# Kernel tuning notes

Measured on AMD Instinct MI355X. Metric: run time of the kernel, lower is better.

Reference implementation:

```python
import jax, jax.numpy as jnp
import numpy as np

N_NODES = 100000
N_EDGES = 1600000
N_GRAPHS = 100
DIMS = [128, 128, 118, 103, 5]  # in_feats, h, h-10, h-25, num_classes


def setup_inputs() -> dict:
    key = jax.random.key(0)
    ks = jax.random.split(key, 16)
    inp = {
        "in_feat": jax.random.normal(ks[0], (N_NODES, DIMS[0]), dtype=jnp.float32),
        "src": jax.random.randint(ks[1], (N_EDGES,), 0, N_NODES, dtype=jnp.int32),
        "dst": jax.random.randint(ks[2], (N_EDGES,), 0, N_NODES, dtype=jnp.int32),
        "graph_ids": (jnp.arange(N_NODES, dtype=jnp.int32) // (N_NODES // N_GRAPHS)),
    }
    # SAGEConv params: fc_self (no bias), fc_neigh (no bias), shared bias
    for l in range(4):
        din, dout = DIMS[l], DIMS[l + 1]
        inp[f"ws{l+1}"] = jax.random.normal(ks[3 + 3 * l], (din, dout), dtype=jnp.float32) * 0.05
        inp[f"wn{l+1}"] = jax.random.normal(ks[4 + 3 * l], (din, dout), dtype=jnp.float32) * 0.05
        inp[f"b{l+1}"] = jnp.zeros((dout,), dtype=jnp.float32)
    return inp


def reference(in_feat, src, dst, graph_ids,
              ws1, wn1, b1, ws2, wn2, b2, ws3, wn3, b3, ws4, wn4, b4):
    N = in_feat.shape[0]
    # in-degree per dst node, clamped to 1 (DGL: degs.clamp(min=1))
    deg = jnp.clip(jax.ops.segment_sum(jnp.ones((src.shape[0],), in_feat.dtype), dst,
                                       num_segments=N), 1.0, None)

    def sage(h, ws, wn, b):
        # mean-aggregate neighbor features: gather over src, scatter-add to dst
        agg = jax.ops.segment_sum(h[src], dst, num_segments=N) / deg[:, None]
        return h @ ws + agg @ wn + b

    h = jax.nn.relu(sage(in_feat, ws1, wn1, b1))
    h = jax.nn.relu(sage(h, ws2, wn2, b2))
    h = jax.nn.relu(sage(h, ws3, wn3, b3))
    h = sage(h, ws4, wn4, b4)

    # dgl.mean_nodes: per-graph mean pooling over nodes
    ones = jnp.ones((N,), h.dtype)
    cnt = jax.ops.segment_sum(ones, graph_ids, num_segments=N_GRAPHS)
    pooled = jax.ops.segment_sum(h, graph_ids, num_segments=N_GRAPHS) / cnt[:, None]
    return pooled
```

## Files before the change

### kernel.cpp

```cpp
#include <hip/hip_runtime.h>
#include <cstdint>
#include <cstddef>

typedef unsigned int uint32;
typedef unsigned short ushort16;
typedef __attribute__((ext_vector_type(8))) short short8;
typedef __attribute__((ext_vector_type(4))) float floatx4;

__device__ __forceinline__ ushort16 f2bf(float f) {
    uint32 u = __builtin_bit_cast(uint32, f);
    uint32 r = (u + 0x7fffu + ((u >> 16) & 1u)) >> 16;
    return (ushort16)r;
}
__device__ __forceinline__ float bf2f(ushort16 h) {
    uint32 u = ((uint32)h) << 16;
    return __builtin_bit_cast(float, u);
}

#define PBS 4096

__global__ __launch_bounds__(256) void bucket_hist_kernel(
    const int* __restrict__ dst, int* __restrict__ bcnt, int E, int NBUCK) {
    __shared__ int l[512];
    int t = threadIdx.x;
    for (int b = t; b < NBUCK; b += 256) l[b] = 0;
    __syncthreads();
    int e0 = blockIdx.x * PBS;
    int e1 = e0 + PBS; if (e1 > E) e1 = E;
    for (int j = e0 + t; j < e1; j += 256)
        atomicAdd(&l[dst[j] >> 8], 1);
    __syncthreads();
    for (int b = t; b < NBUCK; b += 256) {
        int c = l[b];
        if (c) atomicAdd(&bcnt[b], c);
    }
}

__global__ __launch_bounds__(256) void bucket_scan_kernel(
    const int* __restrict__ bcnt, int* __restrict__ bucketOff,
    int* __restrict__ cursorA, int NBUCK, int E) {
    __shared__ int a[512], b[512];
    int t = threadIdx.x;
    a[t] = (t < NBUCK) ? bcnt[t] : 0;
    a[t + 256] = (t + 256 < NBUCK) ? bcnt[t + 256] : 0;
    __syncthreads();
    int* cur = a; int* nxt = b;
    for (int o = 1; o < 512; o <<= 1) {
#pragma unroll
        for (int i = t; i < 512; i += 256)
            nxt[i] = cur[i] + ((i >= o) ? cur[i - o] : 0);
        __syncthreads();
        int* tmp = cur; cur = nxt; nxt = tmp;
    }
#pragma unroll
    for (int i = t; i < 512; i += 256) {
        if (i < NBUCK) {
            int off = (i == 0) ? 0 : cur[i - 1];
            bucketOff[i] = off;
            cursorA[i] = off;
        }
    }
    if (t == 0) bucketOff[NBUCK] = E;
}

__global__ __launch_bounds__(256) void bucket_partition_kernel(
    const int* __restrict__ src, const int* __restrict__ dst,
    int* __restrict__ cursorA, uint32* __restrict__ ebuf, int E, int NBUCK) {
    __shared__ int lbase[512];
    int tid = threadIdx.x;
    for (int b = tid; b < NBUCK; b += 256) lbase[b] = 0;
    __syncthreads();
    int e0 = blockIdx.x * PBS;
    int e1 = e0 + PBS; if (e1 > E) e1 = E;
    for (int j = e0 + tid; j < e1; j += 256)
        atomicAdd(&lbase[dst[j] >> 8], 1);
    __syncthreads();
    for (int b = tid; b < NBUCK; b += 256) {
        int c = lbase[b];
        lbase[b] = c ? atomicAdd(&cursorA[b], c) : 0;
    }
    __syncthreads();
    for (int j = e0 + tid; j < e1; j += 256) {
        int d = dst[j];
        int p = atomicAdd(&lbase[d >> 8], 1);
        ebuf[p] = ((uint32)src[j] << 8) | (uint32)(d & 255);
    }
}

__global__ __launch_bounds__(256) void bucket_build_kernel(
    const uint32* __restrict__ ebuf, const int* __restrict__ bucketOff,
    int* __restrict__ row_ptr, float* __restrict__ degf,
    int* __restrict__ csr, int N, int E) {
    __shared__ int ldeg[256];
    __shared__ int lscan[256];
    __shared__ int lcur[256];
    int b = blockIdx.x, t = threadIdx.x;
    int n0 = b << 8;
    int s = bucketOff[b], e = bucketOff[b + 1];
    ldeg[t] = 0;
    __syncthreads();
    for (int j = s + t; j < e; j += 256)
        atomicAdd(&ldeg[ebuf[j] & 255u], 1);
    __syncthreads();
    int v = ldeg[t];
    lscan[t] = v;
    __syncthreads();
    for (int off = 1; off < 256; off <<= 1) {
        int x = (t >= off) ? lscan[t - off] : 0;
        __syncthreads();
        lscan[t] += x;
        __syncthreads();
    }
    int excl = lscan[t] - v;
    int node = n0 + t;
    if (node < N) {
        row_ptr[node] = s + excl;
        degf[node] = (float)(v > 0 ? v : 1);
    }
    lcur[t] = s + excl;
    __syncthreads();
    for (int j = s + t; j < e; j += 256) {
        uint32 en = ebuf[j];
        int p = atomicAdd(&lcur[en & 255u], 1);
        csr[p] = (int)(en >> 8);
    }
    if (b == 0 && t == 0) row_ptr[N] = E;
}

__global__ void conv_bf16_kernel(const float* __restrict__ x, ushort16* __restrict__ y, int n8) {
    int i = blockIdx.x * blockDim.x + threadIdx.x;
    if (i >= n8) return;
    const float4 a = *(const float4*)(x + (size_t)i * 8);
    const float4 b = *(const float4*)(x + (size_t)i * 8 + 4);
    uint4 o;
    o.x = (uint32)f2bf(a.x) | ((uint32)f2bf(a.y) << 16);
    o.y = (uint32)f2bf(a.z) | ((uint32)f2bf(a.w) << 16);
    o.z = (uint32)f2bf(b.x) | ((uint32)f2bf(b.y) << 16);
    o.w = (uint32)f2bf(b.z) | ((uint32)f2bf(b.w) << 16);
    *(uint4*)(y + (size_t)i * 8) = o;
}

__global__ void prep_w_all_kernel(
    const float* __restrict__ W0s, const float* __restrict__ W0n,
    const float* __restrict__ W1s, const float* __restrict__ W1n,
    const float* __restrict__ W2s, const float* __restrict__ W2n,
    ushort16* __restrict__ Whi, ushort16* __restrict__ Wlo) {
    int mat = blockIdx.x >> 6;
    int idx = (blockIdx.x & 63) * 256 + threadIdx.x;
    const float* Wt[6] = {W0s, W0n, W1s, W1n, W2s, W2n};
    const int Kt[6] = {128, 128, 128, 128, 118, 118};
    const int Mt[6] = {128, 128, 118, 118, 103, 103};
    int n = idx >> 7, k = idx & 127;
    int K = Kt[mat], M = Mt[mat];
    float w = (k < K && n < M) ? Wt[mat][(size_t)k * M + n] : 0.f;
    ushort16 h = f2bf(w);
    float lo = w - bf2f(h);
    Whi[(size_t)mat * 16384 + idx] = h;
    Wlo[(size_t)mat * 16384 + idx] = f2bf(lo);
}

template<int UNROLL>
__global__ __launch_bounds__(256) void aggregate_pre_kernel(
    const ushort16* __restrict__ h,
    const int* __restrict__ row_ptr, const int* __restrict__ csr,
    const float* __restrict__ degf, ushort16* __restrict__ aggH, int N) {
    int wid = threadIdx.x >> 6;
    int lane = threadIdx.x & 63;
    int node = blockIdx.x * 4 + wid;
    if (node >= N) return;
    int s = row_ptr[node], e = row_ptr[node + 1];
    int c = lane & 15;
    int eo = lane >> 4;
    float aLo[4] = {}, aHi[4] = {};
    int j = s + eo;
    for (; j + (UNROLL - 1) * 4 < e; j += UNROLL * 4) {
        uint4 v[UNROLL];
#pragma unroll
        for (int u = 0; u < UNROLL; ++u) {
            int src_n = csr[j + u * 4];
            v[u] = *(const uint4*)(h + ((size_t)src_n << 7) + (c << 3));
        }
#pragma unroll
        for (int u = 0; u < UNROLL; ++u) {
            uint32 w[4] = {v[u].x, v[u].y, v[u].z, v[u].w};
#pragma unroll
            for (int p = 0; p < 4; ++p) {
                aLo[p] += __builtin_bit_cast(float, w[p] << 16);
                aHi[p] += __builtin_bit_cast(float, w[p] & 0xffff0000u);
            }
        }
    }
    for (; j + 4 < e; j += 8) {
        int s0 = csr[j];
        int s1 = csr[j + 4];
        uint4 v0 = *(const uint4*)(h + ((size_t)s0 << 7) + (c << 3));
        uint4 v1 = *(const uint4*)(h + ((size_t)s1 << 7) + (c << 3));
        uint32 w0[4] = {v0.x, v0.y, v0.z, v0.w};
        uint32 w1[4] = {v1.x, v1.y, v1.z, v1.w};
#pragma unroll
        for (int p = 0; p < 4; ++p) {
            aLo[p] += __builtin_bit_cast(float, w0[p] << 16);
            aHi[p] += __builtin_bit_cast(float, w0[p] & 0xffff0000u);
            aLo[p] += __builtin_bit_cast(float, w1[p] << 16);
            aHi[p] += __builtin_bit_cast(float, w1[p] & 0xffff0000u);
        }
    }
    for (; j < e; j += 4) {
        int src_n = csr[j];
        uint4 v = *(const uint4*)(h + ((size_t)src_n << 7) + (c << 3));
        uint32 w[4] = {v.x, v.y, v.z, v.w};
#pragma unroll
        for (int p = 0; p < 4; ++p) {
            aLo[p] += __builtin_bit_cast(float, w[p] << 16);
            aHi[p] += __builtin_bit_cast(float, w[p] & 0xffff0000u);
        }
    }
#pragma unroll
    for (int m = 16; m < 64; m <<= 1) {
#pragma unroll
        for (int p = 0; p < 4; ++p) {
            aLo[p] += __shfl_xor(aLo[p], m, 64);
            aHi[p] += __shfl_xor(aHi[p], m, 64);
        }
    }
    if (lane < 16) {
        float inv = 1.f / degf[node];
        uint4 ov;
        ov.x = (uint32)f2bf(aLo[0] * inv) | ((uint32)f2bf(aHi[0] * inv) << 16);
        ov.y = (uint32)f2bf(aLo[1] * inv) | ((uint32)f2bf(aHi[1] * inv) << 16);
        ov.z = (uint32)f2bf(aLo[2] * inv) | ((uint32)f2bf(aHi[2] * inv) << 16);
        ov.w = (uint32)f2bf(aLo[3] * inv) | ((uint32)f2bf(aHi[3] * inv) << 16);
        *(uint4*)(aggH + ((size_t)node << 7) + (c << 3)) = ov;
    }
}

#define RS 40
__global__ __launch_bounds__(256) void mfma_fused_kernel(
    const ushort16* __restrict__ A, const ushort16* __restrict__ G,
    const ushort16* __restrict__ Whi, const ushort16* __restrict__ Wlo,
    const float* __restrict__ bias,
    ushort16* __restrict__ Out, int N, int M) {
    __shared__ ushort16 Bs[4][64 * RS];
    const int tid = threadIdx.x;
    const int wave = tid >> 6;
    const int lane = tid & 63;
    const int quad = lane >> 4;
    const int m16 = lane & 15;
    const ushort16* Wg[4] = {Whi, Wlo, Whi + 16384, Wlo + 16384};

    floatx4 acc[4] = {};

    const int n0 = blockIdx.y * 64;
    int rowA = blockIdx.x * 64 + wave * 16 + m16;
    if (rowA >= N) rowA = N - 1;
    const ushort16* Arow = A + (size_t)rowA * 128;
    const ushort16* Grow = G + (size_t)rowA * 128;

    const int sn = tid >> 2, sh = tid & 3;
    for (int k0 = 0; k0 < 128; k0 += 32) {
#pragma unroll
        for (int mat = 0; mat < 4; ++mat) {
            const ushort16* g = Wg[mat] + (size_t)(n0 + sn) * 128 + k0 + sh * 8;
            *(uint4*)(&Bs[mat][sn * RS + sh * 8]) = *(const uint4*)g;
        }
        short8 af = *(const short8*)(Arow + k0 + quad * 8);
        short8 gf = *(const short8*)(Grow + k0 + quad * 8);
        __syncthreads();
#pragma unroll
        for (int t = 0; t < 4; ++t) {
            int nb = t * 16 + m16;
            short8 bsh = *(const short8*)(&Bs[0][nb * RS + quad * 8]);
            short8 bsl = *(const short8*)(&Bs[1][nb * RS + quad * 8]);
            short8 bnh = *(const short8*)(&Bs[2][nb * RS + quad * 8]);
            short8 bnl = *(const short8*)(&Bs[3][nb * RS + quad * 8]);
            acc[t] = __builtin_amdgcn_mfma_f32_16x16x32_bf16(af, bsh, acc[t], 0, 0, 0);
            acc[t] = __builtin_amdgcn_mfma_f32_16x16x32_bf16(gf, bnh, acc[t], 0, 0, 0);
            acc[t] = __builtin_amdgcn_mfma_f32_16x16x32_bf16(af, bsl, acc[t], 0, 0, 0);
            acc[t] = __builtin_amdgcn_mfma_f32_16x16x32_bf16(gf, bnl, acc[t], 0, 0, 0);
        }
        __syncthreads();
    }

    int rowBase = blockIdx.x * 64 + wave * 16 + quad * 4;
#pragma unroll
    for (int t = 0; t < 4; ++t) {
        int colt = n0 + t * 16 + m16;
        bool inc = (colt < M);
        float b = inc ? bias[colt] : 0.f;
#pragma unroll
        for (int r = 0; r < 4; ++r) {
            int row = rowBase + r;
            if (row < N) {
                float v = inc ? fmaxf(acc[t][r] + b, 0.f) : 0.f;
                Out[(size_t)row * 128 + colt] = f2bf(v);
            }
        }
    }
}

__global__ __launch_bounds__(256) void gemm4_kernel(
    const ushort16* __restrict__ A, const float* __restrict__ ws,
    const float* __restrict__ wn, const float* __restrict__ b4,
    float* __restrict__ Cs, float* __restrict__ Cn, int N, int K, int M) {
    __shared__ float Wsh[520], Wnh[520];
    int tid = threadIdx.x;
    for (int i = tid; i < K * M; i += 256) { Wsh[i] = ws[i]; Wnh[i] = wn[i]; }
    __syncthreads();
    int node = blockIdx.x * 256 + tid;
    if (node >= N) return;
    const ushort16* row = A + ((size_t)node << 7);
    float s[5] = {}, n[5] = {};
    for (int c8 = 0; c8 * 8 < K; ++c8) {
        uint4 v = *(const uint4*)(row + c8 * 8);
        uint32 w[4] = {v.x, v.y, v.z, v.w};
#pragma unroll
        for (int j = 0; j < 8; ++j) {
            int k = c8 * 8 + j;
            if (k < K) {
                float a = (j & 1) ? __builtin_bit_cast(float, w[j >> 1] & 0xffff0000u)
                                  : __builtin_bit_cast(float, w[j >> 1] << 16);
#pragma unroll
                for (int m = 0; m < 5; ++m) {
                    s[m] += a * Wsh[k * 5 + m];
                    n[m] += a * Wnh[k * 5 + m];
                }
            }
        }
    }
    size_t o = (size_t)node * 8;
#pragma unroll
    for (int m = 0; m < 5; ++m) {
        Cs[o + m] = s[m] + b4[m];
        Cn[o + m] = n[m];
    }
#pragma unroll
    for (int m = 5; m < 8; ++m) { Cs[o + m] = 0.f; Cn[o + m] = 0.f; }
}

template<int CPW, int UNROLL, int SLOG>
__global__ __launch_bounds__(256) void aggregate_fp32_kernel(
    const float* __restrict__ hs, const float* __restrict__ hn,
    const int* __restrict__ row_ptr, const int* __restrict__ csr,
    const float* __restrict__ degf, float* __restrict__ out, int N) {
    constexpr int EPI = 64 / CPW;
    int wid = threadIdx.x >> 6;
    int lane = threadIdx.x & 63;
    int node = blockIdx.x * 4 + wid;
    if (node >= N) return;
    int s = row_ptr[node], e = row_ptr[node + 1];
    int c = lane & (CPW - 1);
    int eo = lane / CPW;
    float4 acc = make_float4(0.f, 0.f, 0.f, 0.f);
    int j = s + eo;
    for (; j + (UNROLL - 1) * EPI < e; j += UNROLL * EPI) {
        float4 v[UNROLL];
#pragma unroll
        for (int u = 0; u < UNROLL; ++u) {
            int src_n = csr[j + u * EPI];
            v[u] = *(const float4*)(hn + ((size_t)src_n << SLOG) + (c << 2));
        }
#pragma unroll
        for (int u = 0; u < UNROLL; ++u) {
            acc.x += v[u].x; acc.y += v[u].y; acc.z += v[u].z; acc.w += v[u].w;
        }
    }
    for (; j < e; j += EPI) {
        int src_n = csr[j];
        float4 v = *(const float4*)(hn + ((size_t)src_n << SLOG) + (c << 2));
        acc.x += v.x; acc.y += v.y; acc.z += v.z; acc.w += v.w;
    }
#pragma unroll
    for (int m = CPW; m < 64; m <<= 1) {
        acc.x += __shfl_xor(acc.x, m, 64);
        acc.y += __shfl_xor(acc.y, m, 64);
        acc.z += __shfl_xor(acc.z, m, 64);
        acc.w += __shfl_xor(acc.w, m, 64);
    }
    if (lane < CPW) {
        float d = 1.f / degf[node];
        size_t o = ((size_t)node << SLOG) + (lane << 2);
        float4 hv = *(const float4*)(hs + o);
        float4 r;
        r.x = hv.x + acc.x * d;
        r.y = hv.y + acc.y * d;
        r.z = hv.z + acc.z * d;
        r.w = hv.w + acc.w * d;
        *(float4*)(out + o) = r;
    }
}

__global__ __launch_bounds__(256) void pool_kernel(
    const float* __restrict__ h, float* __restrict__ out, int npg) {
    __shared__ float sh[4][5];
    int g = blockIdx.x;
    int t = threadIdx.x;
    float acc[5] = {0.f, 0.f, 0.f, 0.f, 0.f};
    int base = g * npg;
    for (int i = t; i < npg; i += 256) {
        const float* r = h + ((size_t)(base + i) << 3);
#pragma unroll
        for (int f = 0; f < 5; ++f) acc[f] += r[f];
    }
#pragma unroll
    for (int off = 32; off > 0; off >>= 1) {
#pragma unroll
        for (int f = 0; f < 5; ++f) acc[f] += __shfl_down(acc[f], off, 64);
    }
    int wid = t >> 6, lane = t & 63;
    if (lane == 0) {
#pragma unroll
        for (int f = 0; f < 5; ++f) sh[wid][f] = acc[f];
    }
    __syncthreads();
    if (t == 0) {
        float inv = 1.f / (float)npg;
#pragma unroll
        for (int f = 0; f < 5; ++f)
            out[g * 5 + f] = (sh[0][f] + sh[1][f] + sh[2][f] + sh[3][f]) * inv;
    }
}

extern "C" void kernel_launch(void* const* d_in, const int* in_sizes, int n_in,
                              void* d_out, int out_size, void* d_ws, size_t ws_size,
                              hipStream_t stream) {
    const float* in_feat = (const float*)d_in[0];
    const int* src = (const int*)d_in[1];
    const int* dst = (const int*)d_in[2];
    const int DIMS[5] = {128, 128, 118, 103, 5};
    const int N = in_sizes[0] / 128;
    const int E = in_sizes[1];
    const int G = out_size / 5;
    const int NBUCK = (N + 255) >> 8;

    char* base = (char*)d_ws;
    size_t off = 0;
    auto carve = [&](size_t bytes) -> void* {
        off = (off + 255) & ~(size_t)255;
        void* p = base + off;
        off += bytes;
        return p;
    };
    int* bcnt = (int*)carve((size_t)NBUCK * 4);
    int* bucketOff = (int*)carve((size_t)(NBUCK + 1) * 4);
    int* cursorA = (int*)carve((size_t)NBUCK * 4);
    int* row_ptr = (int*)carve((size_t)(N + 1) * 4);
    float* degf = (float*)carve((size_t)N * 4);
    uint32* ebuf = (uint32*)carve((size_t)E * 4);
    int* csr = (int*)carve((size_t)E * 4);
    ushort16* buf0 = (ushort16*)carve((size_t)(N + 256) * 128 * 2);
    ushort16* buf1 = (ushort16*)carve((size_t)(N + 256) * 128 * 2);
    ushort16* aggH = (ushort16*)carve((size_t)(N + 256) * 128 * 2);
    ushort16* Whi = (ushort16*)carve((size_t)6 * 16384 * 2);
    ushort16* Wlo = (ushort16*)carve((size_t)6 * 16384 * 2);
    float* Cs4 = (float*)carve((size_t)N * 8 * 4);
    float* Cn4 = (float*)carve((size_t)N * 8 * 4);
    float* out4 = (float*)carve((size_t)N * 8 * 4);
    (void)n_in; (void)ws_size;

    hipMemsetAsync(bcnt, 0, (size_t)NBUCK * 4, stream);
    bucket_hist_kernel<<<(E + PBS - 1) / PBS, 256, 0, stream>>>(dst, bcnt, E, NBUCK);
    bucket_scan_kernel<<<1, 256, 0, stream>>>(bcnt, bucketOff, cursorA, NBUCK, E);
    bucket_partition_kernel<<<(E + PBS - 1) / PBS, 256, 0, stream>>>(
        src, dst, cursorA, ebuf, E, NBUCK);
    bucket_build_kernel<<<NBUCK, 256, 0, stream>>>(
        ebuf, bucketOff, row_ptr, degf, csr, N, E);

    int n8 = N * 16;
    conv_bf16_kernel<<<(n8 + 255) / 256, 256, 0, stream>>>(in_feat, buf0, n8);
    prep_w_all_kernel<<<6 * 64, 256, 0, stream>>>(
        (const float*)d_in[4], (const float*)d_in[5],
        (const float*)d_in[7], (const float*)d_in[8],
        (const float*)d_in[10], (const float*)d_in[11],
        Whi, Wlo);

    ushort16* hb[4] = {buf0, buf1, buf0, buf1};
    dim3 ggrid((N + 63) / 64, 2);
    for (int l = 0; l < 3; ++l) {
        int M = DIMS[l + 1];
        const float* b = (const float*)d_in[6 + 3 * l];
        aggregate_pre_kernel<4><<<(N + 3) / 4, 256, 0, stream>>>(
            hb[l], row_ptr, csr, degf, aggH, N);
        mfma_fused_kernel<<<ggrid, 256, 0, stream>>>(
            hb[l], aggH, Whi + (size_t)l * 2 * 16384, Wlo + (size_t)l * 2 * 16384,
            b, hb[l + 1], N, M);
    }

    gemm4_kernel<<<(N + 255) / 256, 256, 0, stream>>>(
        hb[3], (const float*)d_in[13], (const float*)d_in[14], (const float*)d_in[15],
        Cs4, Cn4, N, DIMS[3], DIMS[4]);
    aggregate_fp32_kernel<2, 1, 3><<<(N + 3) / 4, 256, 0, stream>>>(
        Cs4, Cn4, row_ptr, csr, degf, out4, N);
    pool_kernel<<<G, 256, 0, stream>>>(out4, (float*)d_out, N / G);
}
```

Before: 516.6 us.

## Preload A/G fragments and stage weights in two K-halves with packed float2 accumulation

```diff
diff --git a/kernel.cpp b/kernel.cpp
--- a/kernel.cpp
+++ b/kernel.cpp
@@ -6,6 +6,8 @@
 typedef unsigned short ushort16;
 typedef __attribute__((ext_vector_type(8))) short short8;
 typedef __attribute__((ext_vector_type(4))) float floatx4;
+typedef __attribute__((ext_vector_type(2))) float float2v;
+typedef __attribute__((ext_vector_type(2))) uint32 uint2v;
 
 __device__ __forceinline__ ushort16 f2bf(float f) {
     uint32 u = __builtin_bit_cast(uint32, f);
@@ -171,7 +173,7 @@
     int s = row_ptr[node], e = row_ptr[node + 1];
     int c = lane & 15;
     int eo = lane >> 4;
-    float aLo[4] = {}, aHi[4] = {};
+    float2v acc2[4] = {};
     int j = s + eo;
     for (; j + (UNROLL - 1) * 4 < e; j += UNROLL * 4) {
         uint4 v[UNROLL];
@@ -185,8 +187,8 @@
             uint32 w[4] = {v[u].x, v[u].y, v[u].z, v[u].w};
 #pragma unroll
             for (int p = 0; p < 4; ++p) {
-                aLo[p] += __builtin_bit_cast(float, w[p] << 16);
-                aHi[p] += __builtin_bit_cast(float, w[p] & 0xffff0000u);
+                uint2v b; b.x = w[p] << 16; b.y = w[p] & 0xffff0000u;
+                acc2[p] += __builtin_bit_cast(float2v, b);
             }
         }
     }
@@ -199,10 +201,10 @@
         uint32 w1[4] = {v1.x, v1.y, v1.z, v1.w};
 #pragma unroll
         for (int p = 0; p < 4; ++p) {
-            aLo[p] += __builtin_bit_cast(float, w0[p] << 16);
-            aHi[p] += __builtin_bit_cast(float, w0[p] & 0xffff0000u);
-            aLo[p] += __builtin_bit_cast(float, w1[p] << 16);
-            aHi[p] += __builtin_bit_cast(float, w1[p] & 0xffff0000u);
+            uint2v b0; b0.x = w0[p] << 16; b0.y = w0[p] & 0xffff0000u;
+            acc2[p] += __builtin_bit_cast(float2v, b0);
+            uint2v b1; b1.x = w1[p] << 16; b1.y = w1[p] & 0xffff0000u;
+            acc2[p] += __builtin_bit_cast(float2v, b1);
         }
     }
     for (; j < e; j += 4) {
@@ -211,36 +213,36 @@
         uint32 w[4] = {v.x, v.y, v.z, v.w};
 #pragma unroll
         for (int p = 0; p < 4; ++p) {
-            aLo[p] += __builtin_bit_cast(float, w[p] << 16);
-            aHi[p] += __builtin_bit_cast(float, w[p] & 0xffff0000u);
+            uint2v b; b.x = w[p] << 16; b.y = w[p] & 0xffff0000u;
+            acc2[p] += __builtin_bit_cast(float2v, b);
         }
     }
 #pragma unroll
     for (int m = 16; m < 64; m <<= 1) {
 #pragma unroll
         for (int p = 0; p < 4; ++p) {
-            aLo[p] += __shfl_xor(aLo[p], m, 64);
-            aHi[p] += __shfl_xor(aHi[p], m, 64);
+            acc2[p].x += __shfl_xor(acc2[p].x, m, 64);
+            acc2[p].y += __shfl_xor(acc2[p].y, m, 64);
         }
     }
     if (lane < 16) {
         float inv = 1.f / degf[node];
         uint4 ov;
-        ov.x = (uint32)f2bf(aLo[0] * inv) | ((uint32)f2bf(aHi[0] * inv) << 16);
-        ov.y = (uint32)f2bf(aLo[1] * inv) | ((uint32)f2bf(aHi[1] * inv) << 16);
-        ov.z = (uint32)f2bf(aLo[2] * inv) | ((uint32)f2bf(aHi[2] * inv) << 16);
-        ov.w = (uint32)f2bf(aLo[3] * inv) | ((uint32)f2bf(aHi[3] * inv) << 16);
+        ov.x = (uint32)f2bf(acc2[0].x * inv) | ((uint32)f2bf(acc2[0].y * inv) << 16);
+        ov.y = (uint32)f2bf(acc2[1].x * inv) | ((uint32)f2bf(acc2[1].y * inv) << 16);
+        ov.z = (uint32)f2bf(acc2[2].x * inv) | ((uint32)f2bf(acc2[2].y * inv) << 16);
+        ov.w = (uint32)f2bf(acc2[3].x * inv) | ((uint32)f2bf(acc2[3].y * inv) << 16);
         *(uint4*)(aggH + ((size_t)node << 7) + (c << 3)) = ov;
     }
 }
 
-#define RS 40
+#define WRS 72
 __global__ __launch_bounds__(256) void mfma_fused_kernel(
     const ushort16* __restrict__ A, const ushort16* __restrict__ G,
     const ushort16* __restrict__ Whi, const ushort16* __restrict__ Wlo,
     const float* __restrict__ bias,
     ushort16* __restrict__ Out, int N, int M) {
-    __shared__ ushort16 Bs[4][64 * RS];
+    __shared__ ushort16 Bs[4][64 * WRS];
     const int tid = threadIdx.x;
     const int wave = tid >> 6;
     const int lane = tid & 63;
@@ -248,37 +250,51 @@
     const int m16 = lane & 15;
     const ushort16* Wg[4] = {Whi, Wlo, Whi + 16384, Wlo + 16384};
 
-    floatx4 acc[4] = {};
-
     const int n0 = blockIdx.y * 64;
     int rowA = blockIdx.x * 64 + wave * 16 + m16;
     if (rowA >= N) rowA = N - 1;
     const ushort16* Arow = A + (size_t)rowA * 128;
     const ushort16* Grow = G + (size_t)rowA * 128;
 
-    const int sn = tid >> 2, sh = tid & 3;
-    for (int k0 = 0; k0 < 128; k0 += 32) {
+    short8 af[4], gf[4];
+#pragma unroll
+    for (int ks = 0; ks < 4; ++ks) {
+        af[ks] = *(const short8*)(Arow + ks * 32 + quad * 8);
+        gf[ks] = *(const short8*)(Grow + ks * 32 + quad * 8);
+    }
+
+    floatx4 acc[4] = {};
+#pragma unroll
+    for (int hf = 0; hf < 2; ++hf) {
+        if (hf) __syncthreads();
 #pragma unroll
         for (int mat = 0; mat < 4; ++mat) {
-            const ushort16* g = Wg[mat] + (size_t)(n0 + sn) * 128 + k0 + sh * 8;
-            *(uint4*)(&Bs[mat][sn * RS + sh * 8]) = *(const uint4*)g;
-        }
-        short8 af = *(const short8*)(Arow + k0 + quad * 8);
-        short8 gf = *(const short8*)(Grow + k0 + quad * 8);
+#pragma unroll
+            for (int i = 0; i < 2; ++i) {
+                int idx = i * 256 + tid;
+                int row = idx >> 3, q = idx & 7;
+                *(uint4*)(&Bs[mat][row * WRS + q * 8]) =
+                    *(const uint4*)(Wg[mat] + (size_t)(n0 + row) * 128 + hf * 64 + q * 8);
+            }
+        }
         __syncthreads();
 #pragma unroll
-        for (int t = 0; t < 4; ++t) {
-            int nb = t * 16 + m16;
-            short8 bsh = *(const short8*)(&Bs[0][nb * RS + quad * 8]);
-            short8 bsl = *(const short8*)(&Bs[1][nb * RS + quad * 8]);
-            short8 bnh = *(const short8*)(&Bs[2][nb * RS + quad * 8]);
-            short8 bnl = *(const short8*)(&Bs[3][nb * RS + quad * 8]);
-            acc[t] = __builtin_amdgcn_mfma_f32_16x16x32_bf16(af, bsh, acc[t], 0, 0, 0);
-            acc[t] = __builtin_amdgcn_mfma_f32_16x16x32_bf16(gf, bnh, acc[t], 0, 0, 0);
-            acc[t] = __builtin_amdgcn_mfma_f32_16x16x32_bf16(af, bsl, acc[t], 0, 0, 0);
-            acc[t] = __builtin_amdgcn_mfma_f32_16x16x32_bf16(gf, bnl, acc[t], 0, 0, 0);
-        }
-        __syncthreads();
+        for (int ks = 0; ks < 2; ++ks) {
+            const int kg = hf * 2 + ks;
+            const int ko = ks * 32 + quad * 8;
+#pragma unroll
+            for (int t = 0; t < 4; ++t) {
+                int nb = t * 16 + m16;
+                short8 bsh = *(const short8*)(&Bs[0][nb * WRS + ko]);
+                short8 bsl = *(const short8*)(&Bs[1][nb * WRS + ko]);
+                short8 bnh = *(const short8*)(&Bs[2][nb * WRS + ko]);
+                short8 bnl = *(const short8*)(&Bs[3][nb * WRS + ko]);
+                acc[t] = __builtin_amdgcn_mfma_f32_16x16x32_bf16(af[kg], bsh, acc[t], 0, 0, 0);
+                acc[t] = __builtin_amdgcn_mfma_f32_16x16x32_bf16(gf[kg], bnh, acc[t], 0, 0, 0);
+                acc[t] = __builtin_amdgcn_mfma_f32_16x16x32_bf16(af[kg], bsl, acc[t], 0, 0, 0);
+                acc[t] = __builtin_amdgcn_mfma_f32_16x16x32_bf16(gf[kg], bnl, acc[t], 0, 0, 0);
+            }
+        }
     }
 
     int rowBase = blockIdx.x * 64 + wave * 16 + quad * 4;
```

Result: slower. 542.1 us (+4.9%).

## Fuse prep kernels into one launch and register-prefetch weight tiles in MFMA GEMM

Applied to the files above, without the earlier changes.

```diff
diff --git a/kernel.cpp b/kernel.cpp
--- a/kernel.cpp
+++ b/kernel.cpp
@@ -18,23 +18,6 @@
 }
 
 #define PBS 4096
-
-__global__ __launch_bounds__(256) void bucket_hist_kernel(
-    const int* __restrict__ dst, int* __restrict__ bcnt, int E, int NBUCK) {
-    __shared__ int l[512];
-    int t = threadIdx.x;
-    for (int b = t; b < NBUCK; b += 256) l[b] = 0;
-    __syncthreads();
-    int e0 = blockIdx.x * PBS;
-    int e1 = e0 + PBS; if (e1 > E) e1 = E;
-    for (int j = e0 + t; j < e1; j += 256)
-        atomicAdd(&l[dst[j] >> 8], 1);
-    __syncthreads();
-    for (int b = t; b < NBUCK; b += 256) {
-        int c = l[b];
-        if (c) atomicAdd(&bcnt[b], c);
-    }
-}
 
 __global__ __launch_bounds__(256) void bucket_scan_kernel(
     const int* __restrict__ bcnt, int* __restrict__ bucketOff,
@@ -127,36 +110,59 @@
     if (b == 0 && t == 0) row_ptr[N] = E;
 }
 
-__global__ void conv_bf16_kernel(const float* __restrict__ x, ushort16* __restrict__ y, int n8) {
-    int i = blockIdx.x * blockDim.x + threadIdx.x;
-    if (i >= n8) return;
-    const float4 a = *(const float4*)(x + (size_t)i * 8);
-    const float4 b = *(const float4*)(x + (size_t)i * 8 + 4);
-    uint4 o;
-    o.x = (uint32)f2bf(a.x) | ((uint32)f2bf(a.y) << 16);
-    o.y = (uint32)f2bf(a.z) | ((uint32)f2bf(a.w) << 16);
-    o.z = (uint32)f2bf(b.x) | ((uint32)f2bf(b.y) << 16);
-    o.w = (uint32)f2bf(b.z) | ((uint32)f2bf(b.w) << 16);
-    *(uint4*)(y + (size_t)i * 8) = o;
-}
-
-__global__ void prep_w_all_kernel(
+__global__ __launch_bounds__(256) void prep_fused_kernel(
+    const int* __restrict__ dst, int* __restrict__ bcnt, int E, int NBUCK, int HB,
+    const float* __restrict__ x, ushort16* __restrict__ y, int n8, int CB,
     const float* __restrict__ W0s, const float* __restrict__ W0n,
     const float* __restrict__ W1s, const float* __restrict__ W1n,
     const float* __restrict__ W2s, const float* __restrict__ W2n,
     ushort16* __restrict__ Whi, ushort16* __restrict__ Wlo) {
-    int mat = blockIdx.x >> 6;
-    int idx = (blockIdx.x & 63) * 256 + threadIdx.x;
-    const float* Wt[6] = {W0s, W0n, W1s, W1n, W2s, W2n};
-    const int Kt[6] = {128, 128, 128, 128, 118, 118};
-    const int Mt[6] = {128, 128, 118, 118, 103, 103};
-    int n = idx >> 7, k = idx & 127;
-    int K = Kt[mat], M = Mt[mat];
-    float w = (k < K && n < M) ? Wt[mat][(size_t)k * M + n] : 0.f;
-    ushort16 h = f2bf(w);
-    float lo = w - bf2f(h);
-    Whi[(size_t)mat * 16384 + idx] = h;
-    Wlo[(size_t)mat * 16384 + idx] = f2bf(lo);
+    __shared__ int l[512];
+    int t = threadIdx.x;
+    int bid = blockIdx.x;
+    if (bid < HB) {
+        for (int b = t; b < NBUCK; b += 256) l[b] = 0;
+        __syncthreads();
+        int e0 = bid * PBS;
+        int e1 = e0 + PBS; if (e1 > E) e1 = E;
+        for (int j = e0 + t; j < e1; j += 256)
+            atomicAdd(&l[dst[j] >> 8], 1);
+        __syncthreads();
+        for (int b = t; b < NBUCK; b += 256) {
+            int c = l[b];
+            if (c) atomicAdd(&bcnt[b], c);
+        }
+        return;
+    }
+    bid -= HB;
+    if (bid < CB) {
+        int i = bid * 256 + t;
+        if (i >= n8) return;
+        const float4 a = *(const float4*)(x + (size_t)i * 8);
+        const float4 b = *(const float4*)(x + (size_t)i * 8 + 4);
+        uint4 o;
+        o.x = (uint32)f2bf(a.x) | ((uint32)f2bf(a.y) << 16);
+        o.y = (uint32)f2bf(a.z) | ((uint32)f2bf(a.w) << 16);
+        o.z = (uint32)f2bf(b.x) | ((uint32)f2bf(b.y) << 16);
+        o.w = (uint32)f2bf(b.z) | ((uint32)f2bf(b.w) << 16);
+        *(uint4*)(y + (size_t)i * 8) = o;
+        return;
+    }
+    bid -= CB;
+    {
+        int mat = bid >> 6;
+        int idx = (bid & 63) * 256 + t;
+        const float* Wt[6] = {W0s, W0n, W1s, W1n, W2s, W2n};
+        const int Kt[6] = {128, 128, 128, 128, 118, 118};
+        const int Mt[6] = {128, 128, 118, 118, 103, 103};
+        int n = idx >> 7, k = idx & 127;
+        int K = Kt[mat], M = Mt[mat];
+        float w = (k < K && n < M) ? Wt[mat][(size_t)k * M + n] : 0.f;
+        ushort16 h = f2bf(w);
+        float lo = w - bf2f(h);
+        Whi[(size_t)mat * 16384 + idx] = h;
+        Wlo[(size_t)mat * 16384 + idx] = f2bf(lo);
+    }
 }
 
 template<int UNROLL>
@@ -257,15 +263,29 @@
     const ushort16* Grow = G + (size_t)rowA * 128;
 
     const int sn = tid >> 2, sh = tid & 3;
+    const ushort16* wb[4];
+#pragma unroll
+    for (int mat = 0; mat < 4; ++mat)
+        wb[mat] = Wg[mat] + (size_t)(n0 + sn) * 128 + sh * 8;
+
+    uint4 st[4];
+#pragma unroll
+    for (int mat = 0; mat < 4; ++mat)
+        st[mat] = *(const uint4*)(wb[mat]);
+
+#pragma unroll
     for (int k0 = 0; k0 < 128; k0 += 32) {
 #pragma unroll
-        for (int mat = 0; mat < 4; ++mat) {
-            const ushort16* g = Wg[mat] + (size_t)(n0 + sn) * 128 + k0 + sh * 8;
-            *(uint4*)(&Bs[mat][sn * RS + sh * 8]) = *(const uint4*)g;
-        }
+        for (int mat = 0; mat < 4; ++mat)
+            *(uint4*)(&Bs[mat][sn * RS + sh * 8]) = st[mat];
         short8 af = *(const short8*)(Arow + k0 + quad * 8);
         short8 gf = *(const short8*)(Grow + k0 + quad * 8);
         __syncthreads();
+        if (k0 < 96) {
+#pragma unroll
+            for (int mat = 0; mat < 4; ++mat)
+                st[mat] = *(const uint4*)(wb[mat] + k0 + 32);
+        }
 #pragma unroll
         for (int t = 0; t < 4; ++t) {
             int nb = t * 16 + m16;
@@ -457,21 +477,22 @@
     float* out4 = (float*)carve((size_t)N * 8 * 4);
     (void)n_in; (void)ws_size;
 
+    int n8 = N * 16;
+    int HB = (E + PBS - 1) / PBS;
+    int CB = (n8 + 255) / 256;
     hipMemsetAsync(bcnt, 0, (size_t)NBUCK * 4, stream);
-    bucket_hist_kernel<<<(E + PBS - 1) / PBS, 256, 0, stream>>>(dst, bcnt, E, NBUCK);
+    prep_fused_kernel<<<HB + CB + 6 * 64, 256, 0, stream>>>(
+        dst, bcnt, E, NBUCK, HB,
+        in_feat, buf0, n8, CB,
+        (const float*)d_in[4], (const float*)d_in[5],
+        (const float*)d_in[7], (const float*)d_in[8],
+        (const float*)d_in[10], (const float*)d_in[11],
+        Whi, Wlo);
     bucket_scan_kernel<<<1, 256, 0, stream>>>(bcnt, bucketOff, cursorA, NBUCK, E);
     bucket_partition_kernel<<<(E + PBS - 1) / PBS, 256, 0, stream>>>(
         src, dst, cursorA, ebuf, E, NBUCK);
     bucket_build_kernel<<<NBUCK, 256, 0, stream>>>(
         ebuf, bucketOff, row_ptr, degf, csr, N, E);
-
-    int n8 = N * 16;
-    conv_bf16_kernel<<<(n8 + 255) / 256, 256, 0, stream>>>(in_feat, buf0, n8);
-    prep_w_all_kernel<<<6 * 64, 256, 0, stream>>>(
-        (const float*)d_in[4], (const float*)d_in[5],
-        (const float*)d_in[7], (const float*)d_in[8],
-        (const float*)d_in[10], (const float*)d_in[11],
-        Whi, Wlo);
 
     ushort16* hb[4] = {buf0, buf1, buf0, buf1};
     dim3 ggrid((N + 63) / 64, 2);
```

Result: slower. 659.4 us (+27.6%).
